# Kernel optimization log

Measured on AMD Instinct MI355X. Metric: run time of the kernel, lower is better.

The kernel has to match this reference:

```python
import jax, jax.numpy as jnp
import numpy as np

TARGET_MAIN_CONTRIBUTION = 0.6
CONTRIB_LOSS_COEF = 0.01
TOP_K = 2
NEG_INF = -1e9


def _gat(x, adj, W1, a1s, a1d, W2, a2s, a2d):
    """Dense 2-layer GAT (pyGAT style): multi-head concat + ELU, then one output head.
    x: [B,S,Fin], adj: [B,S,S], W1: [H,Fin,Fh], a1s/a1d: [H,Fh], W2: [H*Fh,Fout], a2s/a2d: [Fout]."""
    mask = adj > 0  # [B,S,S]
    h = jnp.einsum('bsf,hfo->bhso', x, W1)                      # [B,H,S,Fh]
    es = jnp.einsum('bhso,ho->bhs', h, a1s)
    ed = jnp.einsum('bhso,ho->bhs', h, a1d)
    e = jax.nn.leaky_relu(es[:, :, :, None] + ed[:, :, None, :], 0.2)  # [B,H,S,S]
    att = jax.nn.softmax(jnp.where(mask[:, None], e, NEG_INF), axis=-1)
    h1 = jax.nn.elu(jnp.einsum('bhst,bhto->bhso', att, h))      # [B,H,S,Fh]
    B, H, S, Fh = h1.shape
    h1 = h1.transpose(0, 2, 1, 3).reshape(B, S, H * Fh)         # concat heads
    h2 = h1 @ W2                                                # [B,S,Fout]
    e2 = jax.nn.leaky_relu((h2 @ a2s)[:, :, None] + (h2 @ a2d)[:, None, :], 0.2)
    att2 = jax.nn.softmax(jnp.where(mask, e2, NEG_INF), axis=-1)
    return jnp.einsum('bst,bto->bso', att2, h2)


def setup_inputs() -> dict:
    B, S, D, H, Hd, E = 4, 1024, 256, 6, 64, 3
    key = jax.random.key(0)
    ks = jax.random.split(key, 20)
    feature = jax.random.normal(ks[0], (B, S, D), dtype=jnp.float32)
    # sparse-ish binary adjacency with self-loops
    adj = (jax.random.uniform(ks[1], (B, S, S)) < 0.05).astype(jnp.float32)
    adj = jnp.maximum(adj, jnp.eye(S, dtype=jnp.float32)[None])
    p = lambda k, shape: jax.random.normal(k, shape, dtype=jnp.float32) * 0.1
    return {
        'feature': feature, 'adj': adj,
        'main_W1': p(ks[2], (H, D, Hd)), 'main_a1s': p(ks[3], (H, Hd)), 'main_a1d': p(ks[4], (H, Hd)),
        'main_W2': p(ks[5], (H * Hd, D)), 'main_a2s': p(ks[6], (D,)), 'main_a2d': p(ks[7], (D,)),
        'dep_W1': p(ks[8], (E, H, D, Hd)), 'dep_a1s': p(ks[9], (E, H, Hd)), 'dep_a1d': p(ks[10], (E, H, Hd)),
        'dep_W2': p(ks[11], (E, H * Hd, D)), 'dep_a2s': p(ks[12], (E, D)), 'dep_a2d': p(ks[13], (E, D)),
        'router_W': p(ks[14], (D, E)),
        'blend_W': p(ks[15], (D, D)), 'blend_b': jnp.zeros((D,), dtype=jnp.float32),
        'doc_num': 4, 'sect_num': 32,
    }


def reference(feature, adj, main_W1, main_a1s, main_a1d, main_W2, main_a2s, main_a2d,
              dep_W1, dep_a1s, dep_a1d, dep_W2, dep_a2s, dep_a2d,
              router_W, blend_W, blend_b, doc_num, sect_num):
    B, S, D = feature.shape
    E = router_W.shape[1]
    # main expert on full graph
    main_output = _gat(feature, adj, main_W1, main_a1s, main_a1d, main_W2, main_a2s, main_a2d)
    # per-expert adjacency views (zero out columns by node type)
    col = jnp.arange(S)
    sent_cols = (col < S - sect_num - doc_num).astype(adj.dtype)
    sect_cols = ((col >= S - sect_num - doc_num) & (col < S - doc_num)).astype(adj.dtype)
    doc_cols = (col >= S - doc_num).astype(adj.dtype)
    adj_stack = jnp.stack([adj * sent_cols, adj * sect_cols, adj * doc_cols])  # [E,B,S,S]
    # fixed top-k router
    x_flat = feature.reshape(-1, D)
    gate_probs = jax.nn.softmax(x_flat @ router_W, axis=-1)      # [B*S,E]
    _, top_idx = jax.lax.top_k(gate_probs, TOP_K)                # [B*S,k]
    routing_mask = jax.nn.one_hot(top_idx, E, dtype=feature.dtype).sum(axis=-2)  # [B*S,E] binary
    routing_mask = routing_mask.reshape(B, S, E)
    mask_e = routing_mask.transpose(2, 0, 1)[..., None]          # [E,B,S,1]
    # deputy experts: masked input, masked output, accumulate
    x_e = feature[None] * mask_e                                 # [E,B,S,D]
    dep_out = jax.vmap(_gat)(x_e, adj_stack, dep_W1, dep_a1s, dep_a1d, dep_W2, dep_a2s, dep_a2d)
    deputy_output = (dep_out * mask_e).sum(axis=0)               # [B,S,D]
    # blend gate
    blend_weight = jax.nn.sigmoid(feature @ blend_W + blend_b)
    final_output = blend_weight * main_output + (1.0 - blend_weight) * deputy_output
    main_contribution = blend_weight.mean()
    contribution_loss = jnp.abs(main_contribution - TARGET_MAIN_CONTRIBUTION) * CONTRIB_LOSS_COEF
    return final_output, contribution_loss, main_contribution
```

## Files before the change

### kernel.cpp

```cpp
#include <hip/hip_runtime.h>
#include <math.h>

#define B 4
#define S 1024
#define D 256
#define H 6
#define HD 64
#define NE 3
#define HHD 384
#define ROWS (B*S)
#define MAXN 128

typedef __attribute__((ext_vector_type(8))) short bf8_t;
typedef __attribute__((ext_vector_type(4))) float f32x4;

__device__ __forceinline__ float leaky(float x){ return x > 0.f ? x : 0.2f*x; }

__device__ __forceinline__ unsigned short f2bf(float f){
    union { float f; unsigned int u; } v; v.f = f;
    unsigned int u = v.u;
    return (unsigned short)((u + 0x7FFFu + ((u >> 16) & 1u)) >> 16);
}
__device__ __forceinline__ float bf2f(unsigned short h){
    union { unsigned int u; float f; } v; v.u = ((unsigned int)h) << 16;
    return v.f;
}
__device__ __forceinline__ float blo(unsigned int u){
    union { unsigned int u; float f; } v; v.u = u << 16; return v.f;
}
__device__ __forceinline__ float bhi(unsigned int u){
    union { unsigned int u; float f; } v; v.u = u & 0xffff0000u; return v.f;
}
__device__ __forceinline__ float i2f(int t){
    union { int i; float f; } v; v.i = t; return v.f;
}
__device__ __forceinline__ int f2i(float f){
    union { float f; int i; } v; v.f = f; return v.i;
}

#define PB_CONV   1024
#define PB_NBR    1024
#define PB_W1     1536
#define PB_W2     1536
#define PB_BW      256
#define PB_ZERO    177
#define PB_ROUTER 1024
#define PB_TOTAL  (PB_CONV + PB_NBR + PB_W1 + PB_W2 + PB_BW + PB_ZERO + PB_ROUTER)
#define NZERO     45088

__global__ __launch_bounds__(256) void prep_misc_kernel(
        const float* __restrict__ feature, const float* __restrict__ adj,
        const float* __restrict__ main_W1, const float* __restrict__ dep_W1,
        const float* __restrict__ main_W2, const float* __restrict__ dep_W2,
        const float* __restrict__ blend_W, const float* __restrict__ router_W,
        const int* __restrict__ doc_p, const int* __restrict__ sect_p,
        unsigned short* __restrict__ featbf, short* __restrict__ nbr,
        int4* __restrict__ nbc, unsigned short* __restrict__ w1nk,
        unsigned short* __restrict__ w2nk, unsigned short* __restrict__ bwt,
        float* __restrict__ zbase, float* __restrict__ rmask)
{
    int blk = blockIdx.x, tid = threadIdx.x;
    if (blk < PB_CONV){
        int idx = blk*256 + tid;
        float4 v = ((const float4*)feature)[idx];
        ushort4 o;
        o.x = f2bf(v.x); o.y = f2bf(v.y); o.z = f2bf(v.z); o.w = f2bf(v.w);
        ((ushort4*)featbf)[idx] = o;
        return;
    }
    blk -= PB_CONV;
    if (blk < PB_NBR){
        int wave = tid >> 6, lane = tid & 63;
        int row = blk*4 + wave;
        int b1 = S - *sect_p - *doc_p;
        int b2 = S - *doc_p;
        const float* ar = adj + (size_t)row*S + lane*16;
        float a[16];
        #pragma unroll
        for (int q = 0; q < 4; q++){
            float4 v = ((const float4*)ar)[q];
            a[q*4+0] = v.x; a[q*4+1] = v.y; a[q*4+2] = v.z; a[q*4+3] = v.w;
        }
        int t0 = lane*16;
        int k = 0, c1 = 0, c2 = 0;
        #pragma unroll
        for (int i = 0; i < 16; i++){
            if (a[i] > 0.f){
                k++;
                int t = t0 + i;
                if (t < b1) c1++;
                if (t < b2) c2++;
            }
        }
        int inc = k;
        #pragma unroll
        for (int d = 1; d < 64; d <<= 1){
            int u = __shfl_up(inc, d);
            if (lane >= d) inc += u;
        }
        int off = inc - k;
        int total = __shfl(inc, 63);
        int o = row*MAXN + off;
        #pragma unroll
        for (int i = 0; i < 16; i++){
            if (a[i] > 0.f) nbr[o++] = (short)(t0 + i);
        }
        for (int d = 32; d; d >>= 1){
            c1 += __shfl_down(c1, d);
            c2 += __shfl_down(c2, d);
        }
        if (lane == 0) nbc[row] = make_int4(total, c1, c2, 0);
        return;
    }
    blk -= PB_NBR;
    if (blk < PB_W1){
        int e = blk / 384;
        int idx = (blk - e*384)*256 + tid;
        const float* src = (e == 0) ? main_W1 : dep_W1 + (size_t)(e-1)*H*D*HD;
        int n = idx >> 8, k = idx & 255;
        int h = n >> 6, o = n & 63;
        w1nk[(size_t)e*HHD*D + idx] = f2bf(src[(h*D + k)*HD + o]);
        return;
    }
    blk -= PB_W1;
    if (blk < PB_W2){
        int g = blk*256 + tid;
        int e = g / (D*HHD);
        int rem = g - e*(D*HHD);
        int n = rem / HHD, k = rem - n*HHD;
        const float* src = (e == 0) ? main_W2 : dep_W2 + (size_t)(e-1)*HHD*D;
        w2nk[g] = f2bf(src[k*D + n]);
        return;
    }
    blk -= PB_W2;
    if (blk < PB_BW){
        int col = blk, k = tid;
        bwt[col*D + k] = f2bf(blend_W[k*D + col]);
        return;
    }
    blk -= PB_BW;
    if (blk < PB_ZERO){
        int idx = blk*256 + tid;
        if (idx < NZERO) zbase[idx] = 0.f;
        return;
    }
    blk -= PB_ZERO;
    {
        int wave = tid >> 6, lane = tid & 63;
        int row = blk*4 + wave;
        float4 xv = ((const float4*)(feature + (size_t)row*D))[lane];
        int f = lane*4;
        float xa[4] = {xv.x, xv.y, xv.z, xv.w};
        float p0 = 0.f, p1 = 0.f, p2 = 0.f;
        #pragma unroll
        for (int j = 0; j < 4; j++){
            p0 += xa[j]*router_W[(f+j)*NE + 0];
            p1 += xa[j]*router_W[(f+j)*NE + 1];
            p2 += xa[j]*router_W[(f+j)*NE + 2];
        }
        for (int off = 32; off; off >>= 1){
            p0 += __shfl_down(p0, off);
            p1 += __shfl_down(p1, off);
            p2 += __shfl_down(p2, off);
        }
        if (lane == 0){
            float p[3] = {p0, p1, p2};
            int ex = 0;
            for (int e = 1; e < NE; e++) if (p[e] <= p[ex]) ex = e;
            for (int e = 0; e < NE; e++) rmask[e*ROWS + row] = (e == ex) ? 0.f : 1.f;
        }
    }
}

__global__ __launch_bounds__(256, 4) void gemm1_kernel(const unsigned short* __restrict__ w1nk,
                                                    const unsigned short* __restrict__ featbf,
                                                    const float* __restrict__ rmask,
                                                    const float* __restrict__ main_a1s,
                                                    const float* __restrict__ main_a1d,
                                                    const float* __restrict__ dep_a1s,
                                                    const float* __restrict__ dep_a1d,
                                                    const unsigned short* __restrict__ bwt,
                                                    const float* __restrict__ bb,
                                                    unsigned short* __restrict__ htn4,
                                                    float* __restrict__ es8,
                                                    float* __restrict__ ed8,
                                                    float* __restrict__ meanV1p,
                                                    float* __restrict__ gatebuf,
                                                    float* __restrict__ sumBuf){
    __shared__ float ep[2][64][17];
    int tid = threadIdx.x, wave = tid >> 6, lane = tid & 63;
    int quad = lane >> 4, l16 = lane & 15;
    int e = blockIdx.z;
    int n0 = blockIdx.y*64;

    if (e == 4){
        if (blockIdx.x >= 4) return;
        int m0 = blockIdx.x*64;
        const unsigned short* arow = bwt + (size_t)(m0 + wave*16 + l16)*D + quad*8;
        const unsigned short* brow[4];
        #pragma unroll
        for (int j = 0; j < 4; j++)
            brow[j] = featbf + (size_t)(n0 + j*16 + l16)*D + quad*8;
        f32x4 z4 = {0.f,0.f,0.f,0.f};
        f32x4 acc[4] = {z4, z4, z4, z4};
        bf8_t aF = *(const bf8_t*)(arow);
        bf8_t bF[4];
        #pragma unroll
        for (int j = 0; j < 4; j++) bF[j] = *(const bf8_t*)(brow[j]);
        #pragma unroll
        for (int it = 0; it < D/32; it++){
            bf8_t aC = aF;
            bf8_t bC[4] = {bF[0], bF[1], bF[2], bF[3]};
            if (it + 1 < D/32){
                int kn = (it + 1)*32;
                aF = *(const bf8_t*)(arow + kn);
                #pragma unroll
                for (int j = 0; j < 4; j++) bF[j] = *(const bf8_t*)(brow[j] + kn);
            }
            #pragma unroll
            for (int j = 0; j < 4; j++)
                acc[j] = __builtin_amdgcn_mfma_f32_16x16x32_bf16(aC, bC[j], acc[j], 0, 0, 0);
        }
        int mbase = m0 + wave*16 + quad*4;
        float bias[4];
        #pragma unroll
        for (int r = 0; r < 4; r++) bias[r] = bb[mbase + r];
        float lsum = 0.f;
        #pragma unroll
        for (int j = 0; j < 4; j++){
            int rown = n0 + j*16 + l16;
            f32x4 st;
            #pragma unroll
            for (int r = 0; r < 4; r++){
                float g = 1.f/(1.f + __expf(-(acc[j][r] + bias[r])));
                lsum += g;
                st[r] = g;
            }
            *(f32x4*)(gatebuf + (size_t)rown*D + mbase) = st;
        }
        float* redp = &ep[0][0][0];
        redp[tid] = lsum;
        __syncthreads();
        for (int sft = 128; sft; sft >>= 1){
            if (tid < sft) redp[tid] += redp[tid + sft];
            __syncthreads();
        }
        if (tid == 0) atomicAdd(sumBuf, redp[0]);
        return;
    }

    int m0 = blockIdx.x*64;
    const unsigned short* arow = w1nk + (size_t)e*HHD*D + (size_t)(m0 + wave*16 + l16)*D + quad*8;
    const unsigned short* brow[4];
    bool zr[4];
    #pragma unroll
    for (int j = 0; j < 4; j++){
        int n = n0 + j*16 + l16;
        brow[j] = featbf + (size_t)n*D + quad*8;
        zr[j] = (e > 0) ? (rmask[(size_t)(e-1)*ROWS + n] == 0.f) : false;
    }
    f32x4 z4 = {0.f,0.f,0.f,0.f};
    f32x4 acc[4] = {z4, z4, z4, z4};
    bf8_t bz = {0,0,0,0,0,0,0,0};
    bf8_t aF = *(const bf8_t*)(arow);
    bf8_t bF[4];
    #pragma unroll
    for (int j = 0; j < 4; j++) bF[j] = zr[j] ? bz : *(const bf8_t*)(brow[j]);
    #pragma unroll
    for (int it = 0; it < D/32; it++){
        bf8_t aC = aF;
        bf8_t bC[4] = {bF[0], bF[1], bF[2], bF[3]};
        if (it + 1 < D/32){
            int kn = (it + 1)*32;
            aF = *(const bf8_t*)(arow + kn);
            #pragma unroll
            for (int j = 0; j < 4; j++) bF[j] = zr[j] ? bz : *(const bf8_t*)(brow[j] + kn);
        }
        #pragma unroll
        for (int j = 0; j < 4; j++)
            acc[j] = __builtin_amdgcn_mfma_f32_16x16x32_bf16(aC, bC[j], acc[j], 0, 0, 0);
    }
    int b = n0 >> 10;
    int mbase = m0 + wave*16 + quad*4;
    int obase = wave*16 + quad*4;
    #pragma unroll
    for (int j = 0; j < 4; j++){
        int row = n0 + j*16 + l16;
        ushort4 o;
        o.x = f2bf(acc[j][0]); o.y = f2bf(acc[j][1]);
        o.z = f2bf(acc[j][2]); o.w = f2bf(acc[j][3]);
        *(ushort4*)(htn4 + ((size_t)e*ROWS + row)*HHD + mbase) = o;
    }
    const float* a1sp = (e == 0) ? main_a1s : dep_a1s + (size_t)(e-1)*H*HD;
    const float* a1dp = (e == 0) ? main_a1d : dep_a1d + (size_t)(e-1)*H*HD;
    float a1sv[4], a1dv[4];
    #pragma unroll
    for (int r = 0; r < 4; r++){ a1sv[r] = a1sp[mbase + r]; a1dv[r] = a1dp[mbase + r]; }
    #pragma unroll
    for (int j = 0; j < 4; j++){
        float ps = 0.f, pd = 0.f;
        #pragma unroll
        for (int r = 0; r < 4; r++){ ps += acc[j][r]*a1sv[r]; pd += acc[j][r]*a1dv[r]; }
        ep[0][j*16 + l16][wave*4 + quad] = ps;
        ep[1][j*16 + l16][wave*4 + quad] = pd;
    }
    #pragma unroll
    for (int r = 0; r < 4; r++){
        float cm = acc[0][r] + acc[1][r] + acc[2][r] + acc[3][r];
        for (int off = 8; off; off >>= 1) cm += __shfl_down(cm, off, 16);
        if (l16 == 0)
            atomicAdd(meanV1p + ((size_t)e*B + b)*512 + (obase + r)*8 + blockIdx.x,
                      cm*(1.f/(float)S));
    }
    __syncthreads();
    if (tid < 128){
        int arr = tid >> 6, sl = tid & 63;
        float sum = 0.f;
        #pragma unroll
        for (int i = 0; i < 16; i++) sum += ep[arr][sl][i];
        int n = n0 + sl;
        float* dst = arr ? ed8 : es8;
        dst[(((size_t)e*B + (n >> 10))*S + (n & 1023))*8 + blockIdx.x] = sum;
    }
}

__global__ __launch_bounds__(256) void remap1_kernel(const unsigned short* __restrict__ htn4,
                                                     unsigned short* __restrict__ V1p,
                                                     const int* __restrict__ doc_p,
                                                     const int* __restrict__ sect_p){
    int t = blockIdx.x, b = blockIdx.y, e = blockIdx.z;
    int b1 = S - *sect_p - *doc_p;
    int b2 = S - *doc_p;
    if (e == 1 && t >= b1) return;
    if (e == 2 && (t < b1 || t >= b2)) return;
    if (e == 3 && t < b2) return;
    if (e >= 2 && t < 960) return;
    unsigned short* dst;
    if (e < 2) dst = V1p + ((size_t)(e*B + b)*S + t)*512;
    else       dst = V1p + ((size_t)(2*B)*S + ((size_t)((e-2)*B + b))*64 + (t - 960))*512;
    const unsigned short* src = htn4 + ((size_t)e*ROWS + b*S + t)*HHD;
    int tid = threadIdx.x;
    int c0 = tid*2;
    int o = c0 >> 3, h = c0 & 7;
    unsigned short v0 = (h < 6)   ? src[h*64 + o]       : (unsigned short)0;
    unsigned short v1 = (h+1 < 6) ? src[(h+1)*64 + o]   : (unsigned short)0;
    ushort2 ov; ov.x = v0; ov.y = v1;
    *(ushort2*)(dst + c0) = ov;
}

__global__ __launch_bounds__(256) void attn1_gather_kernel(const unsigned short* __restrict__ V1p,
                                                           const float* __restrict__ es8,
                                                           const float* __restrict__ ed8,
                                                           const short* __restrict__ nbr,
                                                           const int4* __restrict__ nbc,
                                                           const float* __restrict__ meanV1p,
                                                           unsigned short* __restrict__ h1c4){
    __shared__ float wrec[4][MAXN][8];
    int wave = threadIdx.x >> 6, lane = threadIdx.x & 63;
    int s = blockIdx.x*4 + wave;
    int e = blockIdx.y >> 2, b = blockIdx.y & 3;
    int row = b*S + s;
    int4 c = nbc[row];
    int lo = 0, hi = c.x;
    if (e == 1) hi = c.y;
    else if (e == 2){ lo = c.y; hi = c.z; }
    else if (e == 3){ lo = c.z; }
    int nn = hi - lo;
    const float* esp = es8 + (((size_t)e*B + b)*S + s)*8;
    f32x4 es_lo = *(const f32x4*)esp;
    f32x4 es_hi = *(const f32x4*)(esp + 4);
    float esv[6] = {es_lo[0], es_lo[1], es_lo[2], es_lo[3], es_hi[0], es_hi[1]};
    const float* edb = ed8 + (((size_t)e*B + b)*S)*8;
    const short* nl = nbr + (size_t)row*MAXN;
    float w0[6] = {0,0,0,0,0,0}, w1[6] = {0,0,0,0,0,0};
    int t0 = 0, t1 = 0;
    if (lane < nn){
        t0 = nl[lo + lane];
        const float* ep = edb + (size_t)t0*8;
        f32x4 d0 = *(const f32x4*)ep;
        f32x4 d1 = *(const f32x4*)(ep + 4);
        float edv[6] = {d0[0], d0[1], d0[2], d0[3], d1[0], d1[1]};
        #pragma unroll
        for (int h = 0; h < 6; h++) w0[h] = __expf(leaky(esv[h] + edv[h]));
    }
    if (64 + lane < nn){
        t1 = nl[lo + 64 + lane];
        const float* ep = edb + (size_t)t1*8;
        f32x4 d0 = *(const f32x4*)ep;
        f32x4 d1 = *(const f32x4*)(ep + 4);
        float edv[6] = {d0[0], d0[1], d0[2], d0[3], d1[0], d1[1]};
        #pragma unroll
        for (int h = 0; h < 6; h++) w1[h] = __expf(leaky(esv[h] + edv[h]));
    }
    float den[6];
    #pragma unroll
    for (int h = 0; h < 6; h++){
        float d = w0[h] + w1[h];
        for (int o2 = 32; o2; o2 >>= 1) d += __shfl_down(d, o2);
        den[h] = __shfl(d, 0);
    }
    if (lane < nn){
        f32x4 r0 = {w0[0], w0[1], w0[2], w0[3]};
        f32x4 r1 = {w0[4], w0[5], i2f(t0), 0.f};
        *(f32x4*)&wrec[wave][lane][0] = r0;
        *(f32x4*)&wrec[wave][lane][4] = r1;
    }
    if (64 + lane < nn){
        f32x4 r0 = {w1[0], w1[1], w1[2], w1[3]};
        f32x4 r1 = {w1[4], w1[5], i2f(t1), 0.f};
        *(f32x4*)&wrec[wave][64 + lane][0] = r0;
        *(f32x4*)&wrec[wave][64 + lane][4] = r1;
    }
    const unsigned short* Vb;
    int toff;
    if (e < 2){ Vb = V1p + ((size_t)(e*B + b)*S)*512; toff = 0; }
    else      { Vb = V1p + ((size_t)(2*B)*S + ((size_t)((e-2)*B + b))*64)*512; toff = 960; }
    float acc[6] = {0,0,0,0,0,0};
    #pragma unroll 4
    for (int j = 0; j < nn; j++){
        f32x4 r0 = *(const f32x4*)&wrec[wave][j][0];
        f32x4 r1 = *(const f32x4*)&wrec[wave][j][4];
        int t = f2i(r1[2]);
        const unsigned short* vp = Vb + (size_t)(t - toff)*512 + lane*8;
        uint4 dv = *(const uint4*)vp;
        acc[0] += r0[0]*blo(dv.x); acc[1] += r0[1]*bhi(dv.x);
        acc[2] += r0[2]*blo(dv.y); acc[3] += r0[3]*bhi(dv.y);
        acc[4] += r1[0]*blo(dv.z); acc[5] += r1[1]*bhi(dv.z);
    }
    unsigned short* outp = h1c4 + ((size_t)e*ROWS + row)*HHD;
    const float* mv = meanV1p + ((size_t)e*B + b)*512 + lane*8;
    #pragma unroll
    for (int h = 0; h < 6; h++){
        float v = (nn > 0) ? acc[h]/den[h] : mv[h];
        v = v > 0.f ? v : __expf(v) - 1.f;
        outp[h*64 + lane] = f2bf(v);
    }
}

__global__ __launch_bounds__(256, 4) void gemm2_kernel(const unsigned short* __restrict__ w2nk,
                                                    const unsigned short* __restrict__ h1c4,
                                                    const float* __restrict__ main_a2s,
                                                    const float* __restrict__ main_a2d,
                                                    const float* __restrict__ dep_a2s,
                                                    const float* __restrict__ dep_a2d,
                                                    unsigned short* __restrict__ h2n4,
                                                    float* __restrict__ f2s4,
                                                    float* __restrict__ f2d4,
                                                    float* __restrict__ meanV2){
    __shared__ float ep[2][64][17];
    int tid = threadIdx.x, wave = tid >> 6, lane = tid & 63;
    int quad = lane >> 4, l16 = lane & 15;
    int e = blockIdx.z;
    int m0 = blockIdx.x*64;
    int n0 = blockIdx.y*64;
    const unsigned short* arow = w2nk + (size_t)e*D*HHD + (size_t)(m0 + wave*16 + l16)*HHD + quad*8;
    const unsigned short* brow[4];
    #pragma unroll
    for (int j = 0; j < 4; j++)
        brow[j] = h1c4 + (size_t)e*ROWS*HHD + (size_t)(n0 + j*16 + l16)*HHD + quad*8;
    f32x4 z4 = {0.f,0.f,0.f,0.f};
    f32x4 acc[4] = {z4, z4, z4, z4};
    bf8_t aF = *(const bf8_t*)(arow);
    bf8_t bF[4];
    #pragma unroll
    for (int j = 0; j < 4; j++) bF[j] = *(const bf8_t*)(brow[j]);
    #pragma unroll
    for (int it = 0; it < HHD/32; it++){
        bf8_t aC = aF;
        bf8_t bC[4] = {bF[0], bF[1], bF[2], bF[3]};
        if (it + 1 < HHD/32){
            int kn = (it + 1)*32;
            aF = *(const bf8_t*)(arow + kn);
            #pragma unroll
            for (int j = 0; j < 4; j++) bF[j] = *(const bf8_t*)(brow[j] + kn);
        }
        #pragma unroll
        for (int j = 0; j < 4; j++)
            acc[j] = __builtin_amdgcn_mfma_f32_16x16x32_bf16(aC, bC[j], acc[j], 0, 0, 0);
    }
    int b = n0 >> 10;
    int mbase = m0 + wave*16 + quad*4;
    #pragma unroll
    for (int j = 0; j < 4; j++){
        int row = n0 + j*16 + l16;
        ushort4 o;
        o.x = f2bf(acc[j][0]); o.y = f2bf(acc[j][1]);
        o.z = f2bf(acc[j][2]); o.w = f2bf(acc[j][3]);
        *(ushort4*)(h2n4 + ((size_t)e*ROWS + row)*D + mbase) = o;
    }
    const float* a2sp = (e == 0) ? main_a2s : dep_a2s + (size_t)(e-1)*D;
    const float* a2dp = (e == 0) ? main_a2d : dep_a2d + (size_t)(e-1)*D;
    float a2sv[4], a2dv[4];
    #pragma unroll
    for (int r = 0; r < 4; r++){ a2sv[r] = a2sp[mbase + r]; a2dv[r] = a2dp[mbase + r]; }
    #pragma unroll
    for (int j = 0; j < 4; j++){
        float ps = 0.f, pd = 0.f;
        #pragma unroll
        for (int r = 0; r < 4; r++){ ps += acc[j][r]*a2sv[r]; pd += acc[j][r]*a2dv[r]; }
        ep[0][j*16 + l16][wave*4 + quad] = ps;
        ep[1][j*16 + l16][wave*4 + quad] = pd;
    }
    #pragma unroll
    for (int r = 0; r < 4; r++){
        float cm = acc[0][r] + acc[1][r] + acc[2][r] + acc[3][r];
        for (int off = 8; off; off >>= 1) cm += __shfl_down(cm, off, 16);
        if (l16 == 0)
            atomicAdd(meanV2 + ((size_t)e*B + b)*D + mbase + r, cm*(1.f/(float)S));
    }
    __syncthreads();
    if (tid < 128){
        int arr = tid >> 6, sl = tid & 63;
        float sum = 0.f;
        #pragma unroll
        for (int i = 0; i < 16; i++) sum += ep[arr][sl][i];
        int n = n0 + sl;
        float* dst = arr ? f2d4 : f2s4;
        atomicAdd(dst + (size_t)e*ROWS + n, sum);
    }
}

__global__ __launch_bounds__(256) void attn2_blend_kernel(const unsigned short* __restrict__ h2n4,
                                                          const float* __restrict__ f2s4,
                                                          const float* __restrict__ f2d4,
                                                          const short* __restrict__ nbr,
                                                          const int4* __restrict__ nbc,
                                                          const float* __restrict__ meanV2,
                                                          const float* __restrict__ gatebuf,
                                                          const float* __restrict__ rmask,
                                                          const float* __restrict__ sumBuf,
                                                          float* __restrict__ outp){
    __shared__ float2 wrec[4][MAXN];
    __shared__ float outs[4][256];
    int wave = threadIdx.x >> 6, lane = threadIdx.x & 63;
    int s = blockIdx.x, b = blockIdx.y;
    int e = wave;
    int row = b*S + s;
    int4 c = nbc[row];
    int lo = 0, hi = c.x;
    if (e == 1) hi = c.y;
    else if (e == 2){ lo = c.y; hi = c.z; }
    else if (e == 3){ lo = c.z; }
    int nn = hi - lo;
    float fs_r = f2s4[(size_t)e*ROWS + row];
    const float* fdp = f2d4 + (size_t)e*ROWS + b*S;
    const short* nl = nbr + (size_t)row*MAXN;
    float w0 = 0.f, w1 = 0.f;
    int t0 = 0, t1 = 0;
    if (lane < nn){ t0 = nl[lo + lane]; w0 = __expf(leaky(fs_r + fdp[t0])); }
    if (64 + lane < nn){ t1 = nl[lo + 64 + lane]; w1 = __expf(leaky(fs_r + fdp[t1])); }
    float den = w0 + w1;
    for (int o2 = 32; o2; o2 >>= 1) den += __shfl_down(den, o2);
    den = __shfl(den, 0);
    if (lane < nn){ float2 r; r.x = w0; r.y = i2f(t0); wrec[wave][lane] = r; }
    if (64 + lane < nn){ float2 r; r.x = w1; r.y = i2f(t1); wrec[wave][64 + lane] = r; }
    const unsigned short* V = h2n4 + ((size_t)e*ROWS + b*S)*D;
    float acc[4] = {0,0,0,0};
    #pragma unroll 4
    for (int j = 0; j < nn; j++){
        float2 r = wrec[wave][j];
        float w = r.x;
        int t = f2i(r.y);
        const unsigned short* vp = V + (size_t)t*D + lane*4;
        uint2 dv = *(const uint2*)vp;
        acc[0] += w*blo(dv.x); acc[1] += w*bhi(dv.x);
        acc[2] += w*blo(dv.y); acc[3] += w*bhi(dv.y);
    }
    if (nn > 0){
        float inv = 1.f/den;
        #pragma unroll
        for (int q = 0; q < 4; q++) outs[e][lane*4 + q] = acc[q]*inv;
    } else {
        const float* mv = meanV2 + ((size_t)e*B + b)*D + lane*4;
        #pragma unroll
        for (int q = 0; q < 4; q++) outs[e][lane*4 + q] = mv[q];
    }
    __syncthreads();
    int col = threadIdx.x;
    float g = gatebuf[(size_t)row*D + col];
    float rm0 = rmask[row], rm1 = rmask[ROWS + row], rm2 = rmask[2*ROWS + row];
    float dep = rm0*outs[1][col] + rm1*outs[2][col] + rm2*outs[3][col];
    outp[(size_t)row*D + col] = g*outs[0][col] + (1.f - g)*dep;
    if (blockIdx.x == 0 && blockIdx.y == 0 && threadIdx.x == 0){
        float mc = sumBuf[0] / (float)(ROWS*D);
        outp[ROWS*D]     = fabsf(mc - 0.6f)*0.01f;
        outp[ROWS*D + 1] = mc;
    }
}

extern "C" void kernel_launch(void* const* d_in, const int* in_sizes, int n_in,
                              void* d_out, int out_size, void* d_ws, size_t ws_size,
                              hipStream_t stream)
{
    const float* feature  = (const float*)d_in[0];
    const float* adj      = (const float*)d_in[1];
    const float* main_W1  = (const float*)d_in[2];
    const float* main_a1s = (const float*)d_in[3];
    const float* main_a1d = (const float*)d_in[4];
    const float* main_W2  = (const float*)d_in[5];
    const float* main_a2s = (const float*)d_in[6];
    const float* main_a2d = (const float*)d_in[7];
    const float* dep_W1   = (const float*)d_in[8];
    const float* dep_a1s  = (const float*)d_in[9];
    const float* dep_a1d  = (const float*)d_in[10];
    const float* dep_W2   = (const float*)d_in[11];
    const float* dep_a2s  = (const float*)d_in[12];
    const float* dep_a2d  = (const float*)d_in[13];
    const float* router_W = (const float*)d_in[14];
    const float* blend_W  = (const float*)d_in[15];
    const float* blend_b  = (const float*)d_in[16];
    const int*   doc_p    = (const int*)d_in[17];
    const int*   sect_p   = (const int*)d_in[18];

    char* ws = (char*)d_ws;
    size_t off = 0;
    unsigned short* featbf = (unsigned short*)(ws + off); off += (size_t)ROWS*D*2;
    short*          nbr    = (short*)(ws + off);          off += (size_t)ROWS*MAXN*2;
    int4*           nbc    = (int4*)(ws + off);           off += (size_t)ROWS*16;
    unsigned short* w1nk   = (unsigned short*)(ws + off); off += (size_t)4*HHD*D*2;
    unsigned short* w2nk   = (unsigned short*)(ws + off); off += (size_t)4*D*HHD*2;
    unsigned short* bwt    = (unsigned short*)(ws + off); off += (size_t)D*D*2;
    float* es8 = (float*)(ws + off); off += (size_t)4*B*S*8*4;
    float* ed8 = (float*)(ws + off); off += (size_t)4*B*S*8*4;
    float* gatebuf = (float*)(ws + off); off += (size_t)ROWS*D*4;
    unsigned short* htn4 = (unsigned short*)(ws + off); off += (size_t)4*ROWS*HHD*2;
    unsigned short* V1p  = (unsigned short*)(ws + off);
    unsigned short* h2n4 = (unsigned short*)(ws + off);
    {
        size_t v1sz = ((size_t)2*B*S + (size_t)2*B*64)*512*2;
        size_t h2sz = (size_t)4*ROWS*D*2;
        off += (v1sz > h2sz) ? v1sz : h2sz;
    }
    unsigned short* h1c4 = (unsigned short*)(ws + off); off += (size_t)4*ROWS*HHD*2;
    float* f2s4    = (float*)(ws + off); off += (size_t)4*ROWS*4;
    float* f2d4    = (float*)(ws + off); off += (size_t)4*ROWS*4;
    float* meanV1p = (float*)(ws + off); off += (size_t)4*B*512*4;
    float* meanV2  = (float*)(ws + off); off += (size_t)4*B*D*4;
    float* sumBuf  = (float*)(ws + off); off += 128;
    float* rmask   = (float*)(ws + off); off += (size_t)NE*ROWS*4;
    float* outp    = (float*)d_out;

    prep_misc_kernel<<<PB_TOTAL, 256, 0, stream>>>(
        feature, adj, main_W1, dep_W1, main_W2, dep_W2, blend_W, router_W,
        doc_p, sect_p, featbf, nbr, nbc, w1nk, w2nk, bwt, f2s4, rmask);

    gemm1_kernel<<<dim3(H, ROWS/64, 5), 256, 0, stream>>>(w1nk, featbf, rmask,
        main_a1s, main_a1d, dep_a1s, dep_a1d, bwt, blend_b,
        htn4, es8, ed8, meanV1p, gatebuf, sumBuf);
    remap1_kernel<<<dim3(S, B, 4), 256, 0, stream>>>(htn4, V1p, doc_p, sect_p);
    attn1_gather_kernel<<<dim3(S/4, 16), 256, 0, stream>>>(V1p, es8, ed8, nbr, nbc,
        meanV1p, h1c4);
    gemm2_kernel<<<dim3(D/64, ROWS/64, 4), 256, 0, stream>>>(w2nk, h1c4,
        main_a2s, main_a2d, dep_a2s, dep_a2d, h2n4, f2s4, f2d4, meanV2);
    attn2_blend_kernel<<<dim3(S, B), 256, 0, stream>>>(h2n4, f2s4, f2d4, nbr, nbc,
        meanV2, gatebuf, rmask, sumBuf, outp);
}
```

Measured before the change: 234.4 us.

## Fuse remap into gemm1 and compute attention logits via precomputed W1·a vectors

Precomputes per-expert vectors W1·a1s and W1·a1d in the prep kernel so the attention source and destination scores become a small MFMA GEMM of the features against these vectors, computed in a new grid slice. The gemm1 tile is reorganised so each block holds all six heads for 16 output features, letting it write the head-interleaved V1p layout directly and removing the separate remap kernel and the htn4 intermediate buffer. The change drops one launch and a full round trip of the hidden features through global memory. In exchange, the logits are now computed from bf16-rounded projection vectors, which changes rounding slightly, and the output writes are scattered 16-byte stores.

```diff
diff --git a/kernel.cpp b/kernel.cpp
--- a/kernel.cpp
+++ b/kernel.cpp
@@ -43,9 +43,10 @@
 #define PB_W1     1536
 #define PB_W2     1536
 #define PB_BW      256
+#define PB_V1        4
 #define PB_ZERO    177
 #define PB_ROUTER 1024
-#define PB_TOTAL  (PB_CONV + PB_NBR + PB_W1 + PB_W2 + PB_BW + PB_ZERO + PB_ROUTER)
+#define PB_TOTAL  (PB_CONV + PB_NBR + PB_W1 + PB_W2 + PB_BW + PB_V1 + PB_ZERO + PB_ROUTER)
 #define NZERO     45088
 
 __global__ __launch_bounds__(256) void prep_misc_kernel(
@@ -53,11 +54,14 @@
         const float* __restrict__ main_W1, const float* __restrict__ dep_W1,
         const float* __restrict__ main_W2, const float* __restrict__ dep_W2,
         const float* __restrict__ blend_W, const float* __restrict__ router_W,
+        const float* __restrict__ main_a1s, const float* __restrict__ main_a1d,
+        const float* __restrict__ dep_a1s, const float* __restrict__ dep_a1d,
         const int* __restrict__ doc_p, const int* __restrict__ sect_p,
         unsigned short* __restrict__ featbf, short* __restrict__ nbr,
         int4* __restrict__ nbc, unsigned short* __restrict__ w1nk,
         unsigned short* __restrict__ w2nk, unsigned short* __restrict__ bwt,
-        float* __restrict__ zbase, float* __restrict__ rmask)
+        unsigned short* __restrict__ v1, float* __restrict__ zbase,
+        float* __restrict__ rmask)
 {
     int blk = blockIdx.x, tid = threadIdx.x;
     if (blk < PB_CONV){
@@ -139,6 +143,32 @@
         return;
     }
     blk -= PB_BW;
+    if (blk < PB_V1){
+        int e = blk, f = tid;
+        const float* W1src = (e == 0) ? main_W1 : dep_W1 + (size_t)(e-1)*H*D*HD;
+        const float* a1s = (e == 0) ? main_a1s : dep_a1s + (size_t)(e-1)*H*HD;
+        const float* a1d = (e == 0) ? main_a1d : dep_a1d + (size_t)(e-1)*H*HD;
+        #pragma unroll
+        for (int c = 0; c < 16; c++){
+            float acc = 0.f;
+            if (c < 6){
+                int h = c;
+                const float* wr = W1src + (size_t)(h*D + f)*HD;
+                const float* av = a1s + h*HD;
+                #pragma unroll 8
+                for (int o = 0; o < HD; o++) acc += wr[o]*av[o];
+            } else if (c >= 8 && c < 14){
+                int h = c - 8;
+                const float* wr = W1src + (size_t)(h*D + f)*HD;
+                const float* av = a1d + h*HD;
+                #pragma unroll 8
+                for (int o = 0; o < HD; o++) acc += wr[o]*av[o];
+            }
+            v1[((size_t)e*16 + c)*D + f] = f2bf(acc);
+        }
+        return;
+    }
+    blk -= PB_V1;
     if (blk < PB_ZERO){
         int idx = blk*256 + tid;
         if (idx < NZERO) zbase[idx] = 0.f;
@@ -175,33 +205,58 @@
 __global__ __launch_bounds__(256, 4) void gemm1_kernel(const unsigned short* __restrict__ w1nk,
                                                     const unsigned short* __restrict__ featbf,
                                                     const float* __restrict__ rmask,
-                                                    const float* __restrict__ main_a1s,
-                                                    const float* __restrict__ main_a1d,
-                                                    const float* __restrict__ dep_a1s,
-                                                    const float* __restrict__ dep_a1d,
+                                                    const unsigned short* __restrict__ v1,
                                                     const unsigned short* __restrict__ bwt,
                                                     const float* __restrict__ bb,
-                                                    unsigned short* __restrict__ htn4,
-                                                    float* __restrict__ es8,
-                                                    float* __restrict__ ed8,
+                                                    const int* __restrict__ doc_p,
+                                                    const int* __restrict__ sect_p,
+                                                    unsigned short* __restrict__ V1p,
+                                                    float* __restrict__ esed,
                                                     float* __restrict__ meanV1p,
                                                     float* __restrict__ gatebuf,
                                                     float* __restrict__ sumBuf){
-    __shared__ float ep[2][64][17];
+    __shared__ float red[256];
     int tid = threadIdx.x, wave = tid >> 6, lane = tid & 63;
     int quad = lane >> 4, l16 = lane & 15;
     int e = blockIdx.z;
-    int n0 = blockIdx.y*64;
+    f32x4 z4 = {0.f,0.f,0.f,0.f};
+    bf8_t bz = {0,0,0,0,0,0,0,0};
+
+    if (e == 5){
+        int ee = blockIdx.x;
+        int row0 = blockIdx.y*64;
+        int rowA = row0 + wave*16 + l16;
+        bool zrA = (ee > 0) ? (rmask[(size_t)(ee-1)*ROWS + rowA] == 0.f) : false;
+        const unsigned short* arow = featbf + (size_t)rowA*D + quad*8;
+        const unsigned short* brow = v1 + ((size_t)ee*16 + l16)*D + quad*8;
+        f32x4 acc = z4;
+        bf8_t aF = zrA ? bz : *(const bf8_t*)arow;
+        bf8_t bF = *(const bf8_t*)brow;
+        #pragma unroll
+        for (int it = 0; it < D/32; it++){
+            bf8_t aC = aF, bC = bF;
+            if (it + 1 < D/32){
+                int kn = (it + 1)*32;
+                aF = zrA ? bz : *(const bf8_t*)(arow + kn);
+                bF = *(const bf8_t*)(brow + kn);
+            }
+            acc = __builtin_amdgcn_mfma_f32_16x16x32_bf16(aC, bC, acc, 0, 0, 0);
+        }
+        int sbase = row0 + wave*16 + quad*4;
+        #pragma unroll
+        for (int r = 0; r < 4; r++)
+            esed[((size_t)ee*ROWS + sbase + r)*16 + l16] = acc[r];
+        return;
+    }
 
     if (e == 4){
-        if (blockIdx.x >= 4) return;
         int m0 = blockIdx.x*64;
+        int n0 = blockIdx.y*64;
         const unsigned short* arow = bwt + (size_t)(m0 + wave*16 + l16)*D + quad*8;
         const unsigned short* brow[4];
         #pragma unroll
         for (int j = 0; j < 4; j++)
             brow[j] = featbf + (size_t)(n0 + j*16 + l16)*D + quad*8;
-        f32x4 z4 = {0.f,0.f,0.f,0.f};
         f32x4 acc[4] = {z4, z4, z4, z4};
         bf8_t aF = *(const bf8_t*)(arow);
         bf8_t bF[4];
@@ -238,119 +293,82 @@
             }
             *(f32x4*)(gatebuf + (size_t)rown*D + mbase) = st;
         }
-        float* redp = &ep[0][0][0];
-        redp[tid] = lsum;
+        red[tid] = lsum;
         __syncthreads();
         for (int sft = 128; sft; sft >>= 1){
-            if (tid < sft) redp[tid] += redp[tid + sft];
+            if (tid < sft) red[tid] += red[tid + sft];
             __syncthreads();
         }
-        if (tid == 0) atomicAdd(sumBuf, redp[0]);
-        return;
-    }
-
-    int m0 = blockIdx.x*64;
-    const unsigned short* arow = w1nk + (size_t)e*HHD*D + (size_t)(m0 + wave*16 + l16)*D + quad*8;
-    const unsigned short* brow[4];
-    bool zr[4];
-    #pragma unroll
-    for (int j = 0; j < 4; j++){
-        int n = n0 + j*16 + l16;
-        brow[j] = featbf + (size_t)n*D + quad*8;
-        zr[j] = (e > 0) ? (rmask[(size_t)(e-1)*ROWS + n] == 0.f) : false;
-    }
-    f32x4 z4 = {0.f,0.f,0.f,0.f};
-    f32x4 acc[4] = {z4, z4, z4, z4};
-    bf8_t bz = {0,0,0,0,0,0,0,0};
-    bf8_t aF = *(const bf8_t*)(arow);
-    bf8_t bF[4];
-    #pragma unroll
-    for (int j = 0; j < 4; j++) bF[j] = zr[j] ? bz : *(const bf8_t*)(brow[j]);
+        if (tid == 0) atomicAdd(sumBuf, red[0]);
+        return;
+    }
+
+    int og = blockIdx.x;
+    int row0 = blockIdx.y*64;
+    int rowA = row0 + wave*16 + l16;
+    bool zrA = (e > 0) ? (rmask[(size_t)(e-1)*ROWS + rowA] == 0.f) : false;
+    const unsigned short* arow = featbf + (size_t)rowA*D + quad*8;
+    const unsigned short* brow[6];
+    #pragma unroll
+    for (int h = 0; h < 6; h++)
+        brow[h] = w1nk + (size_t)e*HHD*D + (size_t)(h*64 + og*16 + l16)*D + quad*8;
+    f32x4 acc[6] = {z4, z4, z4, z4, z4, z4};
+    bf8_t aF = zrA ? bz : *(const bf8_t*)arow;
+    bf8_t bF[6];
+    #pragma unroll
+    for (int h = 0; h < 6; h++) bF[h] = *(const bf8_t*)(brow[h]);
     #pragma unroll
     for (int it = 0; it < D/32; it++){
         bf8_t aC = aF;
-        bf8_t bC[4] = {bF[0], bF[1], bF[2], bF[3]};
+        bf8_t bC[6] = {bF[0], bF[1], bF[2], bF[3], bF[4], bF[5]};
         if (it + 1 < D/32){
             int kn = (it + 1)*32;
-            aF = *(const bf8_t*)(arow + kn);
+            aF = zrA ? bz : *(const bf8_t*)(arow + kn);
             #pragma unroll
-            for (int j = 0; j < 4; j++) bF[j] = zr[j] ? bz : *(const bf8_t*)(brow[j] + kn);
-        }
-        #pragma unroll
-        for (int j = 0; j < 4; j++)
-            acc[j] = __builtin_amdgcn_mfma_f32_16x16x32_bf16(aC, bC[j], acc[j], 0, 0, 0);
-    }
-    int b = n0 >> 10;
-    int mbase = m0 + wave*16 + quad*4;
-    int obase = wave*16 + quad*4;
-    #pragma unroll
-    for (int j = 0; j < 4; j++){
-        int row = n0 + j*16 + l16;
-        ushort4 o;
-        o.x = f2bf(acc[j][0]); o.y = f2bf(acc[j][1]);
-        o.z = f2bf(acc[j][2]); o.w = f2bf(acc[j][3]);
-        *(ushort4*)(htn4 + ((size_t)e*ROWS + row)*HHD + mbase) = o;
-    }
-    const float* a1sp = (e == 0) ? main_a1s : dep_a1s + (size_t)(e-1)*H*HD;
-    const float* a1dp = (e == 0) ? main_a1d : dep_a1d + (size_t)(e-1)*H*HD;
-    float a1sv[4], a1dv[4];
-    #pragma unroll
-    for (int r = 0; r < 4; r++){ a1sv[r] = a1sp[mbase + r]; a1dv[r] = a1dp[mbase + r]; }
-    #pragma unroll
-    for (int j = 0; j < 4; j++){
-        float ps = 0.f, pd = 0.f;
-        #pragma unroll
-        for (int r = 0; r < 4; r++){ ps += acc[j][r]*a1sv[r]; pd += acc[j][r]*a1dv[r]; }
-        ep[0][j*16 + l16][wave*4 + quad] = ps;
-        ep[1][j*16 + l16][wave*4 + quad] = pd;
-    }
-    #pragma unroll
-    for (int r = 0; r < 4; r++){
-        float cm = acc[0][r] + acc[1][r] + acc[2][r] + acc[3][r];
-        for (int off = 8; off; off >>= 1) cm += __shfl_down(cm, off, 16);
-        if (l16 == 0)
-            atomicAdd(meanV1p + ((size_t)e*B + b)*512 + (obase + r)*8 + blockIdx.x,
-                      cm*(1.f/(float)S));
-    }
-    __syncthreads();
-    if (tid < 128){
-        int arr = tid >> 6, sl = tid & 63;
-        float sum = 0.f;
-        #pragma unroll
-        for (int i = 0; i < 16; i++) sum += ep[arr][sl][i];
-        int n = n0 + sl;
-        float* dst = arr ? ed8 : es8;
-        dst[(((size_t)e*B + (n >> 10))*S + (n & 1023))*8 + blockIdx.x] = sum;
-    }
-}
-
-__global__ __launch_bounds__(256) void remap1_kernel(const unsigned short* __restrict__ htn4,
-                                                     unsigned short* __restrict__ V1p,
-                                                     const int* __restrict__ doc_p,
-                                                     const int* __restrict__ sect_p){
-    int t = blockIdx.x, b = blockIdx.y, e = blockIdx.z;
+            for (int h = 0; h < 6; h++) bF[h] = *(const bf8_t*)(brow[h] + kn);
+        }
+        #pragma unroll
+        for (int h = 0; h < 6; h++)
+            acc[h] = __builtin_amdgcn_mfma_f32_16x16x32_bf16(aC, bC[h], acc[h], 0, 0, 0);
+    }
+    int b = row0 >> 10;
+    int o = og*16 + l16;
+    int tloc = (row0 & 1023) + wave*16 + quad*4;
     int b1 = S - *sect_p - *doc_p;
     int b2 = S - *doc_p;
-    if (e == 1 && t >= b1) return;
-    if (e == 2 && (t < b1 || t >= b2)) return;
-    if (e == 3 && t < b2) return;
-    if (e >= 2 && t < 960) return;
-    unsigned short* dst;
-    if (e < 2) dst = V1p + ((size_t)(e*B + b)*S + t)*512;
-    else       dst = V1p + ((size_t)(2*B)*S + ((size_t)((e-2)*B + b))*64 + (t - 960))*512;
-    const unsigned short* src = htn4 + ((size_t)e*ROWS + b*S + t)*HHD;
-    int tid = threadIdx.x;
-    int c0 = tid*2;
-    int o = c0 >> 3, h = c0 & 7;
-    unsigned short v0 = (h < 6)   ? src[h*64 + o]       : (unsigned short)0;
-    unsigned short v1 = (h+1 < 6) ? src[(h+1)*64 + o]   : (unsigned short)0;
-    ushort2 ov; ov.x = v0; ov.y = v1;
-    *(ushort2*)(dst + c0) = ov;
+    unsigned short* Vslab;
+    if (e < 2) Vslab = V1p + ((size_t)(e*B + b)*S)*512;
+    else       Vslab = V1p + ((size_t)(2*B)*S + ((size_t)((e-2)*B + b))*64)*512;
+    #pragma unroll
+    for (int r = 0; r < 4; r++){
+        int t = tloc + r;
+        bool ok;
+        if (e == 0) ok = true;
+        else if (e == 1) ok = (t < b1);
+        else if (e == 2) ok = (t >= b1) && (t < b2);
+        else ok = (t >= b2);
+        if (ok){
+            int ts = (e < 2) ? t : (t - 960);
+            uint4 pv;
+            pv.x = (unsigned)f2bf(acc[0][r]) | ((unsigned)f2bf(acc[1][r]) << 16);
+            pv.y = (unsigned)f2bf(acc[2][r]) | ((unsigned)f2bf(acc[3][r]) << 16);
+            pv.z = (unsigned)f2bf(acc[4][r]) | ((unsigned)f2bf(acc[5][r]) << 16);
+            pv.w = 0u;
+            *(uint4*)(Vslab + (size_t)ts*512 + o*8) = pv;
+        }
+    }
+    float* mvb = meanV1p + ((size_t)e*B + b)*512;
+    #pragma unroll
+    for (int h = 0; h < 6; h++){
+        float cm = acc[h][0] + acc[h][1] + acc[h][2] + acc[h][3];
+        cm += __shfl_down(cm, 32);
+        cm += __shfl_down(cm, 16);
+        if (quad == 0) atomicAdd(mvb + o*8 + h, cm*(1.f/(float)S));
+    }
 }
 
 __global__ __launch_bounds__(256) void attn1_gather_kernel(const unsigned short* __restrict__ V1p,
-                                                           const float* __restrict__ es8,
-                                                           const float* __restrict__ ed8,
+                                                           const float* __restrict__ esed,
                                                            const short* __restrict__ nbr,
                                                            const int4* __restrict__ nbc,
                                                            const float* __restrict__ meanV1p,
@@ -366,17 +384,17 @@
     else if (e == 2){ lo = c.y; hi = c.z; }
     else if (e == 3){ lo = c.z; }
     int nn = hi - lo;
-    const float* esp = es8 + (((size_t)e*B + b)*S + s)*8;
+    const float* esp = esed + ((size_t)e*ROWS + row)*16;
     f32x4 es_lo = *(const f32x4*)esp;
     f32x4 es_hi = *(const f32x4*)(esp + 4);
     float esv[6] = {es_lo[0], es_lo[1], es_lo[2], es_lo[3], es_hi[0], es_hi[1]};
-    const float* edb = ed8 + (((size_t)e*B + b)*S)*8;
+    const float* edb = esed + ((size_t)e*ROWS + b*S)*16;
     const short* nl = nbr + (size_t)row*MAXN;
     float w0[6] = {0,0,0,0,0,0}, w1[6] = {0,0,0,0,0,0};
     int t0 = 0, t1 = 0;
     if (lane < nn){
         t0 = nl[lo + lane];
-        const float* ep = edb + (size_t)t0*8;
+        const float* ep = edb + (size_t)t0*16 + 8;
         f32x4 d0 = *(const f32x4*)ep;
         f32x4 d1 = *(const f32x4*)(ep + 4);
         float edv[6] = {d0[0], d0[1], d0[2], d0[3], d1[0], d1[1]};
@@ -385,7 +403,7 @@
     }
     if (64 + lane < nn){
         t1 = nl[lo + 64 + lane];
-        const float* ep = edb + (size_t)t1*8;
+        const float* ep = edb + (size_t)t1*16 + 8;
         f32x4 d0 = *(const f32x4*)ep;
         f32x4 d1 = *(const f32x4*)(ep + 4);
         float edv[6] = {d0[0], d0[1], d0[2], d0[3], d1[0], d1[1]};
@@ -620,10 +638,9 @@
     unsigned short* w1nk   = (unsigned short*)(ws + off); off += (size_t)4*HHD*D*2;
     unsigned short* w2nk   = (unsigned short*)(ws + off); off += (size_t)4*D*HHD*2;
     unsigned short* bwt    = (unsigned short*)(ws + off); off += (size_t)D*D*2;
-    float* es8 = (float*)(ws + off); off += (size_t)4*B*S*8*4;
-    float* ed8 = (float*)(ws + off); off += (size_t)4*B*S*8*4;
+    unsigned short* v1     = (unsigned short*)(ws + off); off += (size_t)4*16*D*2;
+    float* esed = (float*)(ws + off); off += (size_t)4*ROWS*16*4;
     float* gatebuf = (float*)(ws + off); off += (size_t)ROWS*D*4;
-    unsigned short* htn4 = (unsigned short*)(ws + off); off += (size_t)4*ROWS*HHD*2;
     unsigned short* V1p  = (unsigned short*)(ws + off);
     unsigned short* h2n4 = (unsigned short*)(ws + off);
     {
@@ -642,13 +659,12 @@
 
     prep_misc_kernel<<<PB_TOTAL, 256, 0, stream>>>(
         feature, adj, main_W1, dep_W1, main_W2, dep_W2, blend_W, router_W,
-        doc_p, sect_p, featbf, nbr, nbc, w1nk, w2nk, bwt, f2s4, rmask);
-
-    gemm1_kernel<<<dim3(H, ROWS/64, 5), 256, 0, stream>>>(w1nk, featbf, rmask,
-        main_a1s, main_a1d, dep_a1s, dep_a1d, bwt, blend_b,
-        htn4, es8, ed8, meanV1p, gatebuf, sumBuf);
-    remap1_kernel<<<dim3(S, B, 4), 256, 0, stream>>>(htn4, V1p, doc_p, sect_p);
-    attn1_gather_kernel<<<dim3(S/4, 16), 256, 0, stream>>>(V1p, es8, ed8, nbr, nbc,
+        main_a1s, main_a1d, dep_a1s, dep_a1d,
+        doc_p, sect_p, featbf, nbr, nbc, w1nk, w2nk, bwt, v1, f2s4, rmask);
+
+    gemm1_kernel<<<dim3(4, ROWS/64, 6), 256, 0, stream>>>(w1nk, featbf, rmask, v1,
+        bwt, blend_b, doc_p, sect_p, V1p, esed, meanV1p, gatebuf, sumBuf);
+    attn1_gather_kernel<<<dim3(S/4, 16), 256, 0, stream>>>(V1p, esed, nbr, nbc,
         meanV1p, h1c4);
     gemm2_kernel<<<dim3(D/64, ROWS/64, 4), 256, 0, stream>>>(w2nk, h1c4,
         main_a2s, main_a2d, dep_a2s, dep_a2d, h2n4, f2s4, f2d4, meanV2);
```

Measured after the change: 263.6 us. 1.12x slower.
